# Optimization experiments

Hardware: AMD Instinct MI355X
Metric: run time of the kernel (lower is better)

The kernel has to match this reference:

```python
import jax, jax.numpy as jnp
import numpy as np

B, S, D, H, K = 16, 2048, 1024, 16, 31  # batch, seq, d_model, n_heads, kernel_size


def setup_inputs() -> dict:
    key = jax.random.key(0)
    ks = jax.random.split(key, 6)
    sc = 1.0 / np.sqrt(D)
    return {
        "query_sequences": jax.random.normal(ks[0], (B, S, D), jnp.float32),
        "key_sequences": jax.random.normal(ks[1], (B, S, D), jnp.float32),
        "value_sequences": jax.random.normal(ks[2], (B, S, D), jnp.float32),
        "key_value_sequence_lengths": jax.random.randint(ks[3], (B,), 1, S + 1, jnp.int32),
        "W_q": jax.random.normal(ks[4], (D, H * K), jnp.float32) * sc,  # cast_queries.weight^T
        "b_q": jnp.zeros((H * K,), jnp.float32),                        # cast_queries.bias
        "conv_bias": jnp.zeros((H,), jnp.float32),
    }


def reference(query_sequences, key_sequences, value_sequences,
              key_value_sequence_lengths, W_q, b_q, conv_bias):
    b, s, d = query_sequences.shape
    h = conv_bias.shape[0]
    k = W_q.shape[1] // h
    r = d // h
    # Generate per-position, per-head depthwise filters from the queries.
    weights = (query_sequences @ W_q + b_q).reshape(b, s, h, k)  # (B,S,H,K)
    # Split key channels into heads and reduce within each head -> (B,S,H)
    ksum = key_sequences.reshape(b, s, h, r).sum(axis=-1)
    pad_l = (k - 1) // 2
    pad_r = k - 1 - pad_l
    kpad = jnp.pad(ksum, ((0, 0), (pad_l, pad_r), (0, 0)))  # (B, S+K-1, H)
    # Cross-correlation with per-position filters:
    # out[b,t,h] = sum_j weights[b,t,h,j] * kpad[b, t+j, h]
    out = jnp.zeros((b, s, h), dtype=weights.dtype)
    for j in range(k):  # fixed small kernel loop
        out = out + weights[..., j] * kpad[:, j:j + s, :]
    out = out + conv_bias  # per-head bias
    return out.transpose(0, 2, 1)  # (B, n_heads, S)
```

## Files before the change

### kernel.cpp

```cpp
#include <hip/hip_runtime.h>
#include <hip/hip_bf16.h>

#define BB 16
#define SS 2048
#define DD 1024
#define HH 16
#define KK 31
#define HK 496

typedef float f32x4 __attribute__((ext_vector_type(4)));
typedef __bf16 bf16x8 __attribute__((ext_vector_type(8)));

__device__ __forceinline__ unsigned short f2bf(float x) {
  unsigned u = __float_as_uint(x);
  unsigned r = u + 0x7FFFu + ((u >> 16) & 1u);
  return (unsigned short)(r >> 16);
}

__device__ __forceinline__ void gll16(const void* g, void* l) {
  __builtin_amdgcn_global_load_lds(
      (const __attribute__((address_space(1))) unsigned int*)g,
      (__attribute__((address_space(3))) unsigned int*)l, 16, 0, 0);
}

__global__ void prep_kernel(const float* __restrict__ Wq,
                            unsigned short* __restrict__ Bimg) {
  int idx = blockIdx.x * 256 + threadIdx.x;
  int e = idx & 7;
  int c = (idx >> 3) & 511;
  int gr = (idx >> 12) & 3;
  int ks = idx >> 14;
  int k = ks * 32 + gr * 8 + e;
  int h = c >> 5, j = c & 31;
  float v = (j < KK) ? Wq[k * HK + h * KK + j] : 0.f;
  Bimg[idx] = f2bf(v);
}

__global__ void ksum_kernel(const float* __restrict__ key,
                            float* __restrict__ ksum) {
  const int row = blockIdx.x;
  const int tid = threadIdx.x;
  const float4 v = reinterpret_cast<const float4*>(key + (size_t)row * DD)[tid];
  float p = v.x + v.y + v.z + v.w;
  p += __shfl_xor(p, 1);
  p += __shfl_xor(p, 2);
  p += __shfl_xor(p, 4);
  p += __shfl_xor(p, 8);
  if ((tid & 15) == 0) ksum[(size_t)row * HH + (tid >> 4)] = p;
}

__global__ __launch_bounds__(512, 4) void mca_kernel(
    const float* __restrict__ q, const float* __restrict__ bq,
    const float* __restrict__ convb, const float* __restrict__ ksum,
    const unsigned short* __restrict__ Bimg, float* __restrict__ out) {
  extern __shared__ char smem[];
  const int tid = threadIdx.x;
  const int w = tid >> 6, lane = tid & 63;
  const int g = lane >> 4, qq = lane & 15;
  const int bid = blockIdx.x;
  const int bb = bid >> 5;
  const int t0 = (bid & 31) << 6;

  char* const bB0 = smem;
  char* const bB1 = smem + 32768;
  char* const bA0 = smem + 65536;
  char* const bA1 = smem + 69632;

  const float* qblk = q + ((size_t)(bb * SS + t0)) * DD;

  f32x4 acc[4][4];
#pragma unroll
  for (int m = 0; m < 4; ++m)
#pragma unroll
    for (int n = 0; n < 4; ++n) acc[m][n] = (f32x4){0.f, 0.f, 0.f, 0.f};

  const int arow = tid >> 3;
  const int apart = tid & 7;
  const int ag = apart >> 1, ah = apart & 1;

  float4 rA;

  auto stageB = [&](char* dst, int ks) {
    const char* src = (const char*)Bimg + (size_t)ks * 32768 + w * 1024 + lane * 16;
    char* d = dst + w * 1024;
#pragma unroll
    for (int rr = 0; rr < 4; ++rr) gll16(src + rr * 8192, d + rr * 8192);
  };

  auto issueA = [&](int ks) {
    rA = *reinterpret_cast<const float4*>(qblk + (size_t)arow * DD + ks * 32 + apart * 4);
  };

  auto writeA = [&](char* dst) {
    unsigned u0 = (unsigned)f2bf(rA.x) | ((unsigned)f2bf(rA.y) << 16);
    unsigned u1 = (unsigned)f2bf(rA.z) | ((unsigned)f2bf(rA.w) << 16);
    *reinterpret_cast<uint2*>(dst + ag * 1024 + arow * 16 + ah * 8) = make_uint2(u0, u1);
  };

  auto computeT = [&](const char* bufA, const char* bufB) {
    bf16x8 af[4], bf[4];
#pragma unroll
    for (int m = 0; m < 4; ++m)
      af[m] = *reinterpret_cast<const bf16x8*>(bufA + g * 1024 + (m * 16 + qq) * 16);
#pragma unroll
    for (int n = 0; n < 4; ++n)
      bf[n] = *reinterpret_cast<const bf16x8*>(bufB + g * 8192 + (w * 64 + n * 16 + qq) * 16);
#pragma unroll
    for (int m = 0; m < 4; ++m)
#pragma unroll
      for (int n = 0; n < 4; ++n)
        acc[m][n] = __builtin_amdgcn_mfma_f32_16x16x32_bf16(af[m], bf[n], acc[m][n], 0, 0, 0);
  };

  issueA(0);
  stageB(bB0, 0);
  writeA(bA0);
  __syncthreads();

  for (int ks = 0; ks < 32; ++ks) {
    char* cA = (ks & 1) ? bA1 : bA0;
    char* cB = (ks & 1) ? bB1 : bB0;
    char* nA = (ks & 1) ? bA0 : bA1;
    char* nB = (ks & 1) ? bB0 : bB1;
    if (ks < 31) {
      issueA(ks + 1);
      stageB(nB, ks + 1);
    }
    computeT(cA, cB);
    if (ks < 31) writeA(nA);
    __syncthreads();
  }

  float bqv[4];
#pragma unroll
  for (int n = 0; n < 4; ++n) {
    int c = w * 64 + n * 16 + qq;
    int h = c >> 5, j = c & 31;
    bqv[n] = (j < KK) ? bq[h * KK + j] : 0.f;
  }
  float cb[2] = {convb[w * 2], convb[w * 2 + 1]};

  float* kl = reinterpret_cast<float*>(smem);
  for (int i = tid; i < 96 * 16; i += 512) {
    int trow = i >> 4, h = i & 15;
    int t = t0 + trow - 15;
    kl[trow * 17 + h] = (t >= 0 && t < SS) ? ksum[((size_t)bb * SS + t) * HH + h] : 0.f;
  }
  __syncthreads();

#pragma unroll
  for (int m = 0; m < 4; ++m) {
    float part[4][2];
#pragma unroll
    for (int r = 0; r < 4; ++r) {
      part[r][0] = 0.f;
      part[r][1] = 0.f;
    }
#pragma unroll
    for (int n = 0; n < 4; ++n) {
      const int hp = n >> 1;
      const int j = (n & 1) * 16 + qq;
      const int h = w * 2 + hp;
#pragma unroll
      for (int r = 0; r < 4; ++r) {
        const int tl = m * 16 + g * 4 + r;
        part[r][hp] += (acc[m][n][r] + bqv[n]) * kl[(tl + j) * 17 + h];
      }
    }
#pragma unroll
    for (int r = 0; r < 4; ++r)
#pragma unroll
      for (int hp = 0; hp < 2; ++hp) {
        float v = part[r][hp];
        v += __shfl_xor(v, 1);
        v += __shfl_xor(v, 2);
        v += __shfl_xor(v, 4);
        v += __shfl_xor(v, 8);
        part[r][hp] = v;
      }
    if (qq < 4) {
      const int r = qq;
      const int t = t0 + m * 16 + g * 4 + r;
#pragma unroll
      for (int hp = 0; hp < 2; ++hp)
        out[((size_t)bb * HH + w * 2 + hp) * SS + t] = part[r][hp] + cb[hp];
    }
  }
}

extern "C" void kernel_launch(void* const* d_in, const int* in_sizes, int n_in,
                              void* d_out, int out_size, void* d_ws, size_t ws_size,
                              hipStream_t stream) {
  const float* q   = (const float*)d_in[0];
  const float* key = (const float*)d_in[1];
  const float* Wq  = (const float*)d_in[4];
  const float* bq  = (const float*)d_in[5];
  const float* cvb = (const float*)d_in[6];
  float* out = (float*)d_out;

  float* ksum = (float*)d_ws;
  unsigned short* Bimg = (unsigned short*)((char*)d_ws + 2097152);

  hipFuncSetAttribute((const void*)mca_kernel,
                      hipFuncAttributeMaxDynamicSharedMemorySize, 73728);

  prep_kernel<<<2048, 256, 0, stream>>>(Wq, Bimg);
  ksum_kernel<<<BB * SS, 256, 0, stream>>>(key, ksum);
  mca_kernel<<<BB * (SS / 64), 512, 73728, stream>>>(q, bq, cvb, ksum, Bimg, out);
}
```

Baseline: 89.16 us.

## Load B fragments directly from global into registers, shrinking LDS to 8KB

Reorders the prepacked bf16 weight image so that each lane's MFMA B fragment is contiguous in global memory. B operands now go straight into registers, double-buffered in software, instead of being staged through 64KB of LDS with global_load_lds. This removes LDS traffic and cuts shared memory from 72KB to 8KB per block, which may allow more resident blocks. In exchange it raises register pressure and relies on L2/cache hits for the weight reloads shared across blocks.

Measured after the change: 79.06 us. 11.3% less time.

```diff
diff --git a/kernel.cpp b/kernel.cpp
--- a/kernel.cpp
+++ b/kernel.cpp
@@ -17,20 +17,17 @@
   return (unsigned short)(r >> 16);
 }
 
-__device__ __forceinline__ void gll16(const void* g, void* l) {
-  __builtin_amdgcn_global_load_lds(
-      (const __attribute__((address_space(1))) unsigned int*)g,
-      (__attribute__((address_space(3))) unsigned int*)l, 16, 0, 0);
-}
-
 __global__ void prep_kernel(const float* __restrict__ Wq,
                             unsigned short* __restrict__ Bimg) {
   int idx = blockIdx.x * 256 + threadIdx.x;
   int e = idx & 7;
-  int c = (idx >> 3) & 511;
-  int gr = (idx >> 12) & 3;
+  int qq = (idx >> 3) & 15;
+  int g = (idx >> 7) & 3;
+  int n = (idx >> 9) & 3;
+  int w = (idx >> 11) & 7;
   int ks = idx >> 14;
-  int k = ks * 32 + gr * 8 + e;
+  int k = ks * 32 + g * 8 + e;
+  int c = w * 64 + n * 16 + qq;
   int h = c >> 5, j = c & 31;
   float v = (j < KK) ? Wq[k * HK + h * KK + j] : 0.f;
   Bimg[idx] = f2bf(v);
@@ -53,7 +50,7 @@
     const float* __restrict__ q, const float* __restrict__ bq,
     const float* __restrict__ convb, const float* __restrict__ ksum,
     const unsigned short* __restrict__ Bimg, float* __restrict__ out) {
-  extern __shared__ char smem[];
+  __shared__ char smem[8192];
   const int tid = threadIdx.x;
   const int w = tid >> 6, lane = tid & 63;
   const int g = lane >> 4, qq = lane & 15;
@@ -61,12 +58,11 @@
   const int bb = bid >> 5;
   const int t0 = (bid & 31) << 6;
 
-  char* const bB0 = smem;
-  char* const bB1 = smem + 32768;
-  char* const bA0 = smem + 65536;
-  char* const bA1 = smem + 69632;
+  char* const bA0 = smem;
+  char* const bA1 = smem + 4096;
 
   const float* qblk = q + ((size_t)(bb * SS + t0)) * DD;
+  const unsigned short* bbase = Bimg + w * 2048 + lane * 8;
 
   f32x4 acc[4][4];
 #pragma unroll
@@ -78,58 +74,63 @@
   const int apart = tid & 7;
   const int ag = apart >> 1, ah = apart & 1;
 
-  float4 rA;
-
-  auto stageB = [&](char* dst, int ks) {
-    const char* src = (const char*)Bimg + (size_t)ks * 32768 + w * 1024 + lane * 16;
-    char* d = dst + w * 1024;
-#pragma unroll
-    for (int rr = 0; rr < 4; ++rr) gll16(src + rr * 8192, d + rr * 8192);
-  };
-
-  auto issueA = [&](int ks) {
+  auto issueA = [&](int ks, float4& rA) {
     rA = *reinterpret_cast<const float4*>(qblk + (size_t)arow * DD + ks * 32 + apart * 4);
   };
-
-  auto writeA = [&](char* dst) {
+  auto writeA = [&](char* dst, const float4& rA) {
     unsigned u0 = (unsigned)f2bf(rA.x) | ((unsigned)f2bf(rA.y) << 16);
     unsigned u1 = (unsigned)f2bf(rA.z) | ((unsigned)f2bf(rA.w) << 16);
     *reinterpret_cast<uint2*>(dst + ag * 1024 + arow * 16 + ah * 8) = make_uint2(u0, u1);
   };
-
-  auto computeT = [&](const char* bufA, const char* bufB) {
-    bf16x8 af[4], bf[4];
+  auto loadB = [&](int ks, bf16x8* pB) {
+    const unsigned short* p = bbase + (size_t)ks * 16384;
+#pragma unroll
+    for (int n = 0; n < 4; ++n)
+      pB[n] = *reinterpret_cast<const bf16x8*>(p + n * 512);
+  };
+  auto computeT = [&](const char* bufA, const bf16x8* pB) {
+    bf16x8 af[4];
 #pragma unroll
     for (int m = 0; m < 4; ++m)
       af[m] = *reinterpret_cast<const bf16x8*>(bufA + g * 1024 + (m * 16 + qq) * 16);
 #pragma unroll
-    for (int n = 0; n < 4; ++n)
-      bf[n] = *reinterpret_cast<const bf16x8*>(bufB + g * 8192 + (w * 64 + n * 16 + qq) * 16);
-#pragma unroll
     for (int m = 0; m < 4; ++m)
 #pragma unroll
       for (int n = 0; n < 4; ++n)
-        acc[m][n] = __builtin_amdgcn_mfma_f32_16x16x32_bf16(af[m], bf[n], acc[m][n], 0, 0, 0);
-  };
-
-  issueA(0);
-  stageB(bB0, 0);
-  writeA(bA0);
-  __syncthreads();
-
-  for (int ks = 0; ks < 32; ++ks) {
-    char* cA = (ks & 1) ? bA1 : bA0;
-    char* cB = (ks & 1) ? bB1 : bB0;
-    char* nA = (ks & 1) ? bA0 : bA1;
-    char* nB = (ks & 1) ? bB0 : bB1;
-    if (ks < 31) {
-      issueA(ks + 1);
-      stageB(nB, ks + 1);
-    }
-    computeT(cA, cB);
-    if (ks < 31) writeA(nA);
-    __syncthreads();
-  }
+        acc[m][n] = __builtin_amdgcn_mfma_f32_16x16x32_bf16(af[m], pB[n], acc[m][n], 0, 0, 0);
+  };
+  auto barrier = [&]() {
+    asm volatile("s_waitcnt lgkmcnt(0)" ::: "memory");
+    __builtin_amdgcn_s_barrier();
+  };
+
+  float4 rA0, rA1;
+  bf16x8 pB_a[4], pB_b[4];
+
+  issueA(0, rA0);
+  loadB(0, pB_a);
+  writeA(bA0, rA0);
+  barrier();
+
+  for (int ks2 = 0; ks2 < 15; ++ks2) {
+    const int ks = ks2 * 2;
+    issueA(ks + 1, rA1);
+    loadB(ks + 1, pB_b);
+    computeT(bA0, pB_a);
+    writeA(bA1, rA1);
+    barrier();
+    issueA(ks + 2, rA0);
+    loadB(ks + 2, pB_a);
+    computeT(bA1, pB_b);
+    writeA(bA0, rA0);
+    barrier();
+  }
+  issueA(31, rA1);
+  loadB(31, pB_b);
+  computeT(bA0, pB_a);
+  writeA(bA1, rA1);
+  barrier();
+  computeT(bA1, pB_b);
 
   float bqv[4];
 #pragma unroll
@@ -140,6 +141,7 @@
   }
   float cb[2] = {convb[w * 2], convb[w * 2 + 1]};
 
+  __syncthreads();
   float* kl = reinterpret_cast<float*>(smem);
   for (int i = tid; i < 96 * 16; i += 512) {
     int trow = i >> 4, h = i & 15;
@@ -201,10 +203,7 @@
   float* ksum = (float*)d_ws;
   unsigned short* Bimg = (unsigned short*)((char*)d_ws + 2097152);
 
-  hipFuncSetAttribute((const void*)mca_kernel,
-                      hipFuncAttributeMaxDynamicSharedMemorySize, 73728);
-
   prep_kernel<<<2048, 256, 0, stream>>>(Wq, Bimg);
   ksum_kernel<<<BB * SS, 256, 0, stream>>>(key, ksum);
-  mca_kernel<<<BB * (SS / 64), 512, 73728, stream>>>(q, bq, cvb, ksum, Bimg, out);
-}
+  mca_kernel<<<BB * (SS / 64), 512, 0, stream>>>(q, bq, cvb, ksum, Bimg, out);
+}
```
